# Kernel optimization log

Measured on AMD Instinct MI355X. Metric: run time of the kernel, lower is better.

## Reference

```python
import jax, jax.numpy as jnp
import numpy as np

N, E, IN_DIM, H, D = 100000, 1600000, 256, 4, 32


def setup_inputs() -> dict:
    key = jax.random.key(0)
    ks = jax.random.split(key, 12)
    glorot = lambda k, shp: jax.random.normal(k, shp, dtype=jnp.float32) * np.float32(np.sqrt(2.0 / (shp[0] + shp[1])))
    return {
        "x": jax.random.normal(ks[0], (N, IN_DIM), dtype=jnp.float32),
        "row": jnp.sort(jax.random.randint(ks[1], (E,), 0, N)),
        "col": jax.random.randint(ks[2], (E,), 0, N),
        "a1_w": glorot(ks[3], (H, IN_DIM)),
        "a1_b": jnp.zeros((H,), jnp.float32),
        "a2_w": glorot(ks[4], (H, IN_DIM)),
        "a2_b": jnp.zeros((H,), jnp.float32),
        "lin_l_w": glorot(ks[5], (H * D, IN_DIM)),
        "lin_l_b": jnp.zeros((H * D,), jnp.float32),
        "lin_r_w": glorot(ks[6], (H * D, IN_DIM)),
        "lin_r_b": jnp.zeros((H * D,), jnp.float32),
    }


def reference(x, row, col, a1_w, a1_b, a2_w, a2_b, lin_l_w, lin_l_b, lin_r_w, lin_r_b):
    n = x.shape[0]
    # per-node attention logits, gathered per edge: attn[e,h] = a1(x)[row[e],h] + a2(x)[col[e],h]
    attn1 = x @ a1_w.T + a1_b            # [N, H]
    attn2 = x @ a2_w.T + a2_b            # [N, H]
    attn = attn1[row] + attn2[col]       # [E, H]
    # segment softmax over destination node (row), numerically stable
    seg_max = jax.ops.segment_max(attn, row, num_segments=n)
    seg_max = jnp.where(jnp.isfinite(seg_max), seg_max, 0.0)  # isolated nodes
    e = jnp.exp(attn - seg_max[row])
    seg_sum = jax.ops.segment_sum(e, row, num_segments=n)
    attn_d = e / (seg_sum[row] + 1e-16)  # [E, H]
    # per-head sparse weighted aggregation: out[r] += attn_d[e] * xw[col[e]]
    xw = (x @ lin_l_w.T + lin_l_b).reshape(n, H, D)
    msg = attn_d[:, :, None] * xw[col]   # [E, H, D]
    out_l = jax.ops.segment_sum(msg, row, num_segments=n).reshape(n, H * D)
    return out_l + x @ lin_r_w.T + lin_r_b
```

## Files before the change

### kernel.cpp

```cpp
#include <hip/hip_runtime.h>
#include <hip/hip_bf16.h>
#include <math.h>

#define IN_DIM 256
#define NH 4
#define HD 128

typedef __attribute__((ext_vector_type(8))) short short8;
typedef __attribute__((ext_vector_type(4))) float floatx4;
typedef __attribute__((ext_vector_type(2))) float floatx2;

__device__ __forceinline__ unsigned short f2bf(float f) {
    __hip_bfloat16 h = __float2bfloat16(f);
    return *reinterpret_cast<unsigned short*>(&h);
}
__device__ __forceinline__ float asf(unsigned int u) {
    union { unsigned int i; float f; } c; c.i = u; return c.f;
}

__global__ __launch_bounds__(256) void setup_k(const float* __restrict__ ll_w,
                                               const float* __restrict__ lr_w,
                                               unsigned short* __restrict__ Wb,
                                               const int* __restrict__ row,
                                               int* __restrict__ rowptr,
                                               int E, int N) {
    if (blockIdx.x < 256) {
        int idx = blockIdx.x * 256 + threadIdx.x;
        int j = idx >> 8, k = idx & 255;
        float v = (j < 128) ? ll_w[(size_t)j * 256 + k] : lr_w[(size_t)(j - 128) * 256 + k];
        Wb[idx] = f2bf(v);
        return;
    }
    int e = (blockIdx.x - 256) * blockDim.x + threadIdx.x;
    if (e >= E) return;
    int r = row[e];
    int rprev = (e > 0) ? row[e - 1] : -1;
    for (int rr = rprev + 1; rr <= r; ++rr) rowptr[rr] = e;
    if (e == E - 1) {
        for (int rr = r + 1; rr <= N; ++rr) rowptr[rr] = E;
    }
}

__global__ __launch_bounds__(512, 2) void node_gemm_k(
    const float* __restrict__ x, const unsigned short* __restrict__ Wb,
    const float* __restrict__ ll_b, const float* __restrict__ lr_b,
    const float* __restrict__ a2_w, const float* __restrict__ a2_b,
    float* __restrict__ eattn,
    unsigned short* __restrict__ xwb, float* __restrict__ out, int N)
{
    __shared__ unsigned short Abuf[32 * 264];
    __shared__ unsigned short LdsX[32 * 136];
    __shared__ float          LdsO[32 * 132];

    const int tid = threadIdx.x;
    const int lane = tid & 63;
    const int w = tid >> 6;
    const int lo = lane & 15;
    const int hi = lane >> 4;

    short8 Bf[2][8];
    int cols[2]; float bias[2];
    #pragma unroll
    for (int ct = 0; ct < 2; ++ct) {
        const int col = w * 32 + ct * 16 + lo;
        cols[ct] = col;
        bias[ct] = (col < HD) ? ll_b[col] : lr_b[col - HD];
        #pragma unroll
        for (int s = 0; s < 8; ++s)
            Bf[ct][s] = *(const short8*)(Wb + (size_t)col * IN_DIM + s * 32 + hi * 8);
    }

    const int tr = tid >> 4;
    const int tq = tid & 15;

    const float ab0 = a2_b[0], ab1 = a2_b[1], ab2 = a2_b[2], ab3 = a2_b[3];

    float4 f0, f1, f2, f3;
    auto gprefetch = [&](int slab) {
        int rg = slab * 32 + tr;
        if (rg >= N) rg = 0;
        const float* px = x + (size_t)rg * IN_DIM + tq * 4;
        f0 = *(const float4*)(px);
        f1 = *(const float4*)(px + 64);
        f2 = *(const float4*)(px + 128);
        f3 = *(const float4*)(px + 192);
    };

    const int nslab = (N + 31) >> 5;
    int slab = blockIdx.x;
    gprefetch(slab);

    for (; slab < nslab; slab += gridDim.x) {
        unsigned short* ab = &Abuf[0];

        {
            ushort4 u;
            u.x = f2bf(f0.x); u.y = f2bf(f0.y); u.z = f2bf(f0.z); u.w = f2bf(f0.w);
            *(ushort4*)(ab + tr * 264 + tq * 4) = u;
            u.x = f2bf(f1.x); u.y = f2bf(f1.y); u.z = f2bf(f1.z); u.w = f2bf(f1.w);
            *(ushort4*)(ab + tr * 264 + 64 + tq * 4) = u;
            u.x = f2bf(f2.x); u.y = f2bf(f2.y); u.z = f2bf(f2.z); u.w = f2bf(f2.w);
            *(ushort4*)(ab + tr * 264 + 128 + tq * 4) = u;
            u.x = f2bf(f3.x); u.y = f2bf(f3.y); u.z = f2bf(f3.z); u.w = f2bf(f3.w);
            *(ushort4*)(ab + tr * 264 + 192 + tq * 4) = u;
        }

        float p0 = 0.f, p1 = 0.f, p2 = 0.f, p3 = 0.f;
        {
            const float* aw = a2_w + tq * 4;
            #pragma unroll
            for (int j = 0; j < 4; ++j) {
                const float4 fx = (j == 0) ? f0 : (j == 1) ? f1 : (j == 2) ? f2 : f3;
                const float4 w0v = *(const float4*)(aw + 0 * IN_DIM + j * 64);
                const float4 w1v = *(const float4*)(aw + 1 * IN_DIM + j * 64);
                const float4 w2v = *(const float4*)(aw + 2 * IN_DIM + j * 64);
                const float4 w3v = *(const float4*)(aw + 3 * IN_DIM + j * 64);
                p0 += fx.x * w0v.x + fx.y * w0v.y + fx.z * w0v.z + fx.w * w0v.w;
                p1 += fx.x * w1v.x + fx.y * w1v.y + fx.z * w1v.z + fx.w * w1v.w;
                p2 += fx.x * w2v.x + fx.y * w2v.y + fx.z * w2v.z + fx.w * w2v.w;
                p3 += fx.x * w3v.x + fx.y * w3v.y + fx.z * w3v.z + fx.w * w3v.w;
            }
        }

        asm volatile("s_waitcnt lgkmcnt(0)\n\ts_barrier" ::: "memory");

        const int next = slab + gridDim.x;
        if (next < nslab) gprefetch(next);

        #pragma unroll
        for (int o = 1; o < 16; o <<= 1) {
            p0 += __shfl_xor(p0, o, 64);
            p1 += __shfl_xor(p1, o, 64);
            p2 += __shfl_xor(p2, o, 64);
            p3 += __shfl_xor(p3, o, 64);
        }
        {
            const int rgo = slab * 32 + tr;
            if (tq == 0 && rgo < N) {
                float4 ev;
                ev.x = __expf(p0 + ab0);
                ev.y = __expf(p1 + ab1);
                ev.z = __expf(p2 + ab2);
                ev.w = __expf(p3 + ab3);
                *(float4*)(eattn + (size_t)rgo * NH) = ev;
            }
        }

        floatx4 acc[2][2];
        #pragma unroll
        for (int rt = 0; rt < 2; ++rt)
            #pragma unroll
            for (int ct = 0; ct < 2; ++ct)
                acc[rt][ct] = (floatx4){0.f, 0.f, 0.f, 0.f};

        #pragma unroll
        for (int s = 0; s < 8; ++s) {
            const short8 A0 = *(const short8*)(ab + lo * 264 + s * 32 + hi * 8);
            const short8 A1 = *(const short8*)(ab + (16 + lo) * 264 + s * 32 + hi * 8);
            acc[0][0] = __builtin_amdgcn_mfma_f32_16x16x32_bf16(A0, Bf[0][s], acc[0][0], 0, 0, 0);
            acc[0][1] = __builtin_amdgcn_mfma_f32_16x16x32_bf16(A0, Bf[1][s], acc[0][1], 0, 0, 0);
            acc[1][0] = __builtin_amdgcn_mfma_f32_16x16x32_bf16(A1, Bf[0][s], acc[1][0], 0, 0, 0);
            acc[1][1] = __builtin_amdgcn_mfma_f32_16x16x32_bf16(A1, Bf[1][s], acc[1][1], 0, 0, 0);
        }

        #pragma unroll
        for (int rt = 0; rt < 2; ++rt)
            #pragma unroll
            for (int ct = 0; ct < 2; ++ct) {
                const int c = cols[ct];
                #pragma unroll
                for (int j = 0; j < 4; ++j) {
                    const int r = rt * 16 + hi * 4 + j;
                    const float v = acc[rt][ct][j] + bias[ct];
                    if (c < HD) LdsX[r * 136 + c] = f2bf(v);
                    else        LdsO[r * 132 + (c - HD)] = v;
                }
            }

        asm volatile("s_waitcnt lgkmcnt(0)\n\ts_barrier" ::: "memory");

        {
            const int rg = slab * 32 + tr;
            if (rg < N) {
                *(uint4*)(xwb + (size_t)rg * HD + tq * 8) =
                    *(const uint4*)(LdsX + tr * 136 + tq * 8);
                float4* od = (float4*)(out + (size_t)rg * HD + tq * 8);
                const float* lsrc = LdsO + tr * 132 + tq * 8;
                od[0] = *(const float4*)(lsrc);
                od[1] = *(const float4*)(lsrc + 4);
            }
        }
    }
}

__global__ __launch_bounds__(256) void edge_aggregate_k(
    const int* __restrict__ rowptr, const int* __restrict__ col,
    const float* __restrict__ eattn,
    const unsigned short* __restrict__ xwb, float* __restrict__ out,
    int N, int E)
{
    const int n = blockIdx.x * 4 + (threadIdx.x >> 6);
    const int lane = threadIdx.x & 63;
    if (n >= N) return;
    const int e0 = __builtin_amdgcn_readfirstlane(rowptr[n]);
    const int e1 = __builtin_amdgcn_readfirstlane(rowptr[n + 1]);
    if (e0 >= e1) return;

    const int h = lane >> 4;
    const int d2 = 2 * lane;
    const int elast = E - 1;

    auto cl = [&](int i) { return col[i <= elast ? i : elast]; };

    floatx2* op = (floatx2*)(out + (size_t)n * HD + d2);
    floatx2 o = __builtin_nontemporal_load(op);

    float s = 0.f, acc0 = 0.f, acc1 = 0.f;
    int e = e0;
    int c[8];
    #pragma unroll
    for (int i = 0; i < 8; ++i) c[i] = cl(e + i);

    for (;;) {
        float wt[8];
        unsigned int pk[8];
        #pragma unroll
        for (int i = 0; i < 8; ++i) wt[i] = eattn[c[i] * NH + h];
        #pragma unroll
        for (int i = 0; i < 8; ++i)
            pk[i] = *(const unsigned int*)(xwb + (size_t)c[i] * HD + d2);
        const int ne = e + 8;
        int nx[8];
        #pragma unroll
        for (int i = 0; i < 8; ++i) nx[i] = cl(ne + i);
        #pragma unroll
        for (int i = 1; i < 8; ++i) wt[i] = (e + i < e1) ? wt[i] : 0.f;
        #pragma unroll
        for (int i = 0; i < 8; ++i) {
            s += wt[i];
            acc0 += wt[i] * asf(pk[i] << 16);
            acc1 += wt[i] * asf(pk[i] & 0xffff0000u);
        }
        if (ne >= e1) break;
        e = ne;
        #pragma unroll
        for (int i = 0; i < 8; ++i) c[i] = nx[i];
    }

    const float inv = 1.f / s;
    o.x += acc0 * inv;
    o.y += acc1 * inv;
    __builtin_nontemporal_store(o, op);
}

extern "C" void kernel_launch(void* const* d_in, const int* in_sizes, int n_in,
                              void* d_out, int out_size, void* d_ws, size_t ws_size,
                              hipStream_t stream) {
    const float* x    = (const float*)d_in[0];
    const int*   row  = (const int*)d_in[1];
    const int*   col  = (const int*)d_in[2];
    const float* a2_w = (const float*)d_in[5];
    const float* a2_b = (const float*)d_in[6];
    const float* ll_w = (const float*)d_in[7];
    const float* ll_b = (const float*)d_in[8];
    const float* lr_w = (const float*)d_in[9];
    const float* lr_b = (const float*)d_in[10];
    float* out = (float*)d_out;

    const int N = in_sizes[0] / IN_DIM;
    const int E = in_sizes[1];

    char* ws = (char*)d_ws;
    size_t off = ((size_t)(N + 1) * sizeof(int) + 255) & ~(size_t)255;
    int*   rowptr = (int*)ws;
    float* eattn  = (float*)(ws + off); off += (size_t)N * NH * sizeof(float);
    unsigned short* xwb = (unsigned short*)(ws + off); off += (size_t)N * HD * sizeof(unsigned short);
    unsigned short* Wb  = (unsigned short*)(ws + off); off += (size_t)256 * IN_DIM * sizeof(unsigned short);

    setup_k<<<256 + (E + 255) / 256, 256, 0, stream>>>(ll_w, lr_w, Wb, row, rowptr, E, N);
    node_gemm_k<<<512, 512, 0, stream>>>(x, Wb, ll_b, lr_b, a2_w, a2_b, eattn, xwb, out, N);
    edge_aggregate_k<<<(N + 3) / 4, 256, 0, stream>>>(rowptr, col, eattn, xwb, out, N, E);
}
```

Measured before the change: 282.9 us.

## Fold setup kernel into node GEMM and reorder MFMA before reductions

Removes the separate setup kernel. Each GEMM block now converts its slice of the fp32 weights to bf16 in registers, and the blocks build rowptr with a grid-stride loop over edges. The MFMA block is moved ahead of the shuffle reduction and the exp store so the two can overlap, and the grid grows from 512 to 768 blocks. This saves a kernel launch and the bf16 weight round-trip through memory. In exchange every block reloads the fp32 weights, and the rowptr loop adds work before the main loop.

Result: slower. 296.2 us (+4.7%).

```diff
diff --git a/kernel.cpp b/kernel.cpp
--- a/kernel.cpp
+++ b/kernel.cpp
@@ -18,35 +18,14 @@
     union { unsigned int i; float f; } c; c.i = u; return c.f;
 }
 
-__global__ __launch_bounds__(256) void setup_k(const float* __restrict__ ll_w,
-                                               const float* __restrict__ lr_w,
-                                               unsigned short* __restrict__ Wb,
-                                               const int* __restrict__ row,
-                                               int* __restrict__ rowptr,
-                                               int E, int N) {
-    if (blockIdx.x < 256) {
-        int idx = blockIdx.x * 256 + threadIdx.x;
-        int j = idx >> 8, k = idx & 255;
-        float v = (j < 128) ? ll_w[(size_t)j * 256 + k] : lr_w[(size_t)(j - 128) * 256 + k];
-        Wb[idx] = f2bf(v);
-        return;
-    }
-    int e = (blockIdx.x - 256) * blockDim.x + threadIdx.x;
-    if (e >= E) return;
-    int r = row[e];
-    int rprev = (e > 0) ? row[e - 1] : -1;
-    for (int rr = rprev + 1; rr <= r; ++rr) rowptr[rr] = e;
-    if (e == E - 1) {
-        for (int rr = r + 1; rr <= N; ++rr) rowptr[rr] = E;
-    }
-}
-
 __global__ __launch_bounds__(512, 2) void node_gemm_k(
-    const float* __restrict__ x, const unsigned short* __restrict__ Wb,
+    const float* __restrict__ x,
+    const float* __restrict__ ll_w, const float* __restrict__ lr_w,
     const float* __restrict__ ll_b, const float* __restrict__ lr_b,
     const float* __restrict__ a2_w, const float* __restrict__ a2_b,
+    const int* __restrict__ row, int* __restrict__ rowptr,
     float* __restrict__ eattn,
-    unsigned short* __restrict__ xwb, float* __restrict__ out, int N)
+    unsigned short* __restrict__ xwb, float* __restrict__ out, int N, int E)
 {
     __shared__ unsigned short Abuf[32 * 264];
     __shared__ unsigned short LdsX[32 * 136];
@@ -58,22 +37,8 @@
     const int lo = lane & 15;
     const int hi = lane >> 4;
 
-    short8 Bf[2][8];
-    int cols[2]; float bias[2];
-    #pragma unroll
-    for (int ct = 0; ct < 2; ++ct) {
-        const int col = w * 32 + ct * 16 + lo;
-        cols[ct] = col;
-        bias[ct] = (col < HD) ? ll_b[col] : lr_b[col - HD];
-        #pragma unroll
-        for (int s = 0; s < 8; ++s)
-            Bf[ct][s] = *(const short8*)(Wb + (size_t)col * IN_DIM + s * 32 + hi * 8);
-    }
-
     const int tr = tid >> 4;
     const int tq = tid & 15;
-
-    const float ab0 = a2_b[0], ab1 = a2_b[1], ab2 = a2_b[2], ab3 = a2_b[3];
 
     float4 f0, f1, f2, f3;
     auto gprefetch = [&](int slab) {
@@ -89,6 +54,39 @@
     const int nslab = (N + 31) >> 5;
     int slab = blockIdx.x;
     gprefetch(slab);
+
+    short8 Bf[2][8];
+    int cols[2]; float bias[2];
+    #pragma unroll
+    for (int ct = 0; ct < 2; ++ct) {
+        const int col = w * 32 + ct * 16 + lo;
+        cols[ct] = col;
+        bias[ct] = (col < HD) ? ll_b[col] : lr_b[col - HD];
+        const float* wsrc = (col < HD) ? (ll_w + (size_t)col * IN_DIM)
+                                       : (lr_w + (size_t)(col - HD) * IN_DIM);
+        #pragma unroll
+        for (int s = 0; s < 8; ++s) {
+            const float4 a = *(const float4*)(wsrc + s * 32 + hi * 8);
+            const float4 b = *(const float4*)(wsrc + s * 32 + hi * 8 + 4);
+            short8 f;
+            f[0] = (short)f2bf(a.x); f[1] = (short)f2bf(a.y);
+            f[2] = (short)f2bf(a.z); f[3] = (short)f2bf(a.w);
+            f[4] = (short)f2bf(b.x); f[5] = (short)f2bf(b.y);
+            f[6] = (short)f2bf(b.z); f[7] = (short)f2bf(b.w);
+            Bf[ct][s] = f;
+        }
+    }
+
+    for (int e = blockIdx.x * 512 + tid; e < E; e += gridDim.x * 512) {
+        const int r = row[e];
+        const int rprev = (e > 0) ? row[e - 1] : -1;
+        for (int rr = rprev + 1; rr <= r; ++rr) rowptr[rr] = e;
+        if (e == E - 1) {
+            for (int rr = r + 1; rr <= N; ++rr) rowptr[rr] = E;
+        }
+    }
+
+    const float ab0 = a2_b[0], ab1 = a2_b[1], ab2 = a2_b[2], ab3 = a2_b[3];
 
     for (; slab < nslab; slab += gridDim.x) {
         unsigned short* ab = &Abuf[0];
@@ -127,6 +125,23 @@
         const int next = slab + gridDim.x;
         if (next < nslab) gprefetch(next);
 
+        floatx4 acc[2][2];
+        #pragma unroll
+        for (int rt = 0; rt < 2; ++rt)
+            #pragma unroll
+            for (int ct = 0; ct < 2; ++ct)
+                acc[rt][ct] = (floatx4){0.f, 0.f, 0.f, 0.f};
+
+        #pragma unroll
+        for (int s = 0; s < 8; ++s) {
+            const short8 A0 = *(const short8*)(ab + lo * 264 + s * 32 + hi * 8);
+            const short8 A1 = *(const short8*)(ab + (16 + lo) * 264 + s * 32 + hi * 8);
+            acc[0][0] = __builtin_amdgcn_mfma_f32_16x16x32_bf16(A0, Bf[0][s], acc[0][0], 0, 0, 0);
+            acc[0][1] = __builtin_amdgcn_mfma_f32_16x16x32_bf16(A0, Bf[1][s], acc[0][1], 0, 0, 0);
+            acc[1][0] = __builtin_amdgcn_mfma_f32_16x16x32_bf16(A1, Bf[0][s], acc[1][0], 0, 0, 0);
+            acc[1][1] = __builtin_amdgcn_mfma_f32_16x16x32_bf16(A1, Bf[1][s], acc[1][1], 0, 0, 0);
+        }
+
         #pragma unroll
         for (int o = 1; o < 16; o <<= 1) {
             p0 += __shfl_xor(p0, o, 64);
@@ -144,23 +159,6 @@
                 ev.w = __expf(p3 + ab3);
                 *(float4*)(eattn + (size_t)rgo * NH) = ev;
             }
-        }
-
-        floatx4 acc[2][2];
-        #pragma unroll
-        for (int rt = 0; rt < 2; ++rt)
-            #pragma unroll
-            for (int ct = 0; ct < 2; ++ct)
-                acc[rt][ct] = (floatx4){0.f, 0.f, 0.f, 0.f};
-
-        #pragma unroll
-        for (int s = 0; s < 8; ++s) {
-            const short8 A0 = *(const short8*)(ab + lo * 264 + s * 32 + hi * 8);
-            const short8 A1 = *(const short8*)(ab + (16 + lo) * 264 + s * 32 + hi * 8);
-            acc[0][0] = __builtin_amdgcn_mfma_f32_16x16x32_bf16(A0, Bf[0][s], acc[0][0], 0, 0, 0);
-            acc[0][1] = __builtin_amdgcn_mfma_f32_16x16x32_bf16(A0, Bf[1][s], acc[0][1], 0, 0, 0);
-            acc[1][0] = __builtin_amdgcn_mfma_f32_16x16x32_bf16(A1, Bf[0][s], acc[1][0], 0, 0, 0);
-            acc[1][1] = __builtin_amdgcn_mfma_f32_16x16x32_bf16(A1, Bf[1][s], acc[1][1], 0, 0, 0);
         }
 
         #pragma unroll
@@ -275,9 +273,8 @@
     int*   rowptr = (int*)ws;
     float* eattn  = (float*)(ws + off); off += (size_t)N * NH * sizeof(float);
     unsigned short* xwb = (unsigned short*)(ws + off); off += (size_t)N * HD * sizeof(unsigned short);
-    unsigned short* Wb  = (unsigned short*)(ws + off); off += (size_t)256 * IN_DIM * sizeof(unsigned short);
-
-    setup_k<<<256 + (E + 255) / 256, 256, 0, stream>>>(ll_w, lr_w, Wb, row, rowptr, E, N);
-    node_gemm_k<<<512, 512, 0, stream>>>(x, Wb, ll_b, lr_b, a2_w, a2_b, eattn, xwb, out, N);
+
+    node_gemm_k<<<768, 512, 0, stream>>>(x, ll_w, lr_w, ll_b, lr_b, a2_w, a2_b,
+                                         row, rowptr, eattn, xwb, out, N, E);
     edge_aggregate_k<<<(N + 3) / 4, 256, 0, stream>>>(rowptr, col, eattn, xwb, out, N, E);
 }
```

## Store lin_r result as bf16 in workspace instead of fp32 to output

Applied to the files above, without the earlier changes.

The GEMM kernel now writes both the lin_l and lin_r projections as bf16 into a combined 256-wide workspace row, instead of writing the lin_r part as fp32 directly to the output. The aggregation kernel reads the bf16 lin_r values for its node and writes the output exactly once, with no read-modify-write. This cuts GEMM store traffic and removes the output read in the edge kernel. In exchange the skip-connection term loses precision to bf16, and gathered xw rows are now strided at 512 bytes instead of 256.

Result: no change. 278.6 us (-1.5%).

```diff
diff --git a/kernel.cpp b/kernel.cpp
--- a/kernel.cpp
+++ b/kernel.cpp
@@ -46,11 +46,10 @@
     const float* __restrict__ ll_b, const float* __restrict__ lr_b,
     const float* __restrict__ a2_w, const float* __restrict__ a2_b,
     float* __restrict__ eattn,
-    unsigned short* __restrict__ xwb, float* __restrict__ out, int N)
+    unsigned short* __restrict__ xwb, int N)
 {
     __shared__ unsigned short Abuf[32 * 264];
-    __shared__ unsigned short LdsX[32 * 136];
-    __shared__ float          LdsO[32 * 132];
+    __shared__ unsigned short LdsE[32 * 264];
 
     const int tid = threadIdx.x;
     const int lane = tid & 63;
@@ -171,9 +170,7 @@
                 #pragma unroll
                 for (int j = 0; j < 4; ++j) {
                     const int r = rt * 16 + hi * 4 + j;
-                    const float v = acc[rt][ct][j] + bias[ct];
-                    if (c < HD) LdsX[r * 136 + c] = f2bf(v);
-                    else        LdsO[r * 132 + (c - HD)] = v;
+                    LdsE[r * 264 + c] = f2bf(acc[rt][ct][j] + bias[ct]);
                 }
             }
 
@@ -182,12 +179,10 @@
         {
             const int rg = slab * 32 + tr;
             if (rg < N) {
-                *(uint4*)(xwb + (size_t)rg * HD + tq * 8) =
-                    *(const uint4*)(LdsX + tr * 136 + tq * 8);
-                float4* od = (float4*)(out + (size_t)rg * HD + tq * 8);
-                const float* lsrc = LdsO + tr * 132 + tq * 8;
-                od[0] = *(const float4*)(lsrc);
-                od[1] = *(const float4*)(lsrc + 4);
+                const uint4* lsrc = (const uint4*)(LdsE + tr * 264 + tq * 16);
+                uint4* dst = (uint4*)(xwb + (size_t)rg * 256 + tq * 16);
+                dst[0] = lsrc[0];
+                dst[1] = lsrc[1];
             }
         }
     }
@@ -204,7 +199,6 @@
     if (n >= N) return;
     const int e0 = __builtin_amdgcn_readfirstlane(rowptr[n]);
     const int e1 = __builtin_amdgcn_readfirstlane(rowptr[n + 1]);
-    if (e0 >= e1) return;
 
     const int h = lane >> 4;
     const int d2 = 2 * lane;
@@ -212,45 +206,55 @@
 
     auto cl = [&](int i) { return col[i <= elast ? i : elast]; };
 
+    const unsigned int lr = *(const unsigned int*)(xwb + (size_t)n * 256 + HD + d2);
+    const float lrx = asf(lr << 16);
+    const float lry = asf(lr & 0xffff0000u);
+
+    float2 o;
+    o.x = lrx; o.y = lry;
+
+    if (e0 < e1) {
+        float s = 0.f, acc0 = 0.f, acc1 = 0.f;
+        int e = e0;
+        int c[8];
+        #pragma unroll
+        for (int i = 0; i < 8; ++i) c[i] = cl(e + i);
+
+        for (;;) {
+            float wt[8];
+            unsigned int pk[8];
+            #pragma unroll
+            for (int i = 0; i < 8; ++i) wt[i] = eattn[c[i] * NH + h];
+            #pragma unroll
+            for (int i = 0; i < 8; ++i)
+                pk[i] = *(const unsigned int*)(xwb + (size_t)c[i] * 256 + d2);
+            const int ne = e + 8;
+            int nx[8];
+            #pragma unroll
+            for (int i = 0; i < 8; ++i) nx[i] = cl(ne + i);
+            #pragma unroll
+            for (int i = 1; i < 8; ++i) wt[i] = (e + i < e1) ? wt[i] : 0.f;
+            #pragma unroll
+            for (int i = 0; i < 8; ++i) {
+                s += wt[i];
+                acc0 += wt[i] * asf(pk[i] << 16);
+                acc1 += wt[i] * asf(pk[i] & 0xffff0000u);
+            }
+            if (ne >= e1) break;
+            e = ne;
+            #pragma unroll
+            for (int i = 0; i < 8; ++i) c[i] = nx[i];
+        }
+
+        const float inv = 1.f / s;
+        o.x += acc0 * inv;
+        o.y += acc1 * inv;
+    }
+
     floatx2* op = (floatx2*)(out + (size_t)n * HD + d2);
-    floatx2 o = __builtin_nontemporal_load(op);
-
-    float s = 0.f, acc0 = 0.f, acc1 = 0.f;
-    int e = e0;
-    int c[8];
-    #pragma unroll
-    for (int i = 0; i < 8; ++i) c[i] = cl(e + i);
-
-    for (;;) {
-        float wt[8];
-        unsigned int pk[8];
-        #pragma unroll
-        for (int i = 0; i < 8; ++i) wt[i] = eattn[c[i] * NH + h];
-        #pragma unroll
-        for (int i = 0; i < 8; ++i)
-            pk[i] = *(const unsigned int*)(xwb + (size_t)c[i] * HD + d2);
-        const int ne = e + 8;
-        int nx[8];
-        #pragma unroll
-        for (int i = 0; i < 8; ++i) nx[i] = cl(ne + i);
-        #pragma unroll
-        for (int i = 1; i < 8; ++i) wt[i] = (e + i < e1) ? wt[i] : 0.f;
-        #pragma unroll
-        for (int i = 0; i < 8; ++i) {
-            s += wt[i];
-            acc0 += wt[i] * asf(pk[i] << 16);
-            acc1 += wt[i] * asf(pk[i] & 0xffff0000u);
-        }
-        if (ne >= e1) break;
-        e = ne;
-        #pragma unroll
-        for (int i = 0; i < 8; ++i) c[i] = nx[i];
-    }
-
-    const float inv = 1.f / s;
-    o.x += acc0 * inv;
-    o.y += acc1 * inv;
-    __builtin_nontemporal_store(o, op);
+    floatx2 ov;
+    ov.x = o.x; ov.y = o.y;
+    __builtin_nontemporal_store(ov, op);
 }
 
 extern "C" void kernel_launch(void* const* d_in, const int* in_sizes, int n_in,
@@ -274,10 +278,10 @@
     size_t off = ((size_t)(N + 1) * sizeof(int) + 255) & ~(size_t)255;
     int*   rowptr = (int*)ws;
     float* eattn  = (float*)(ws + off); off += (size_t)N * NH * sizeof(float);
-    unsigned short* xwb = (unsigned short*)(ws + off); off += (size_t)N * HD * sizeof(unsigned short);
+    unsigned short* xwb = (unsigned short*)(ws + off); off += (size_t)N * 256 * sizeof(unsigned short);
     unsigned short* Wb  = (unsigned short*)(ws + off); off += (size_t)256 * IN_DIM * sizeof(unsigned short);
 
     setup_k<<<256 + (E + 255) / 256, 256, 0, stream>>>(ll_w, lr_w, Wb, row, rowptr, E, N);
-    node_gemm_k<<<512, 512, 0, stream>>>(x, Wb, ll_b, lr_b, a2_w, a2_b, eattn, xwb, out, N);
+    node_gemm_k<<<512, 512, 0, stream>>>(x, Wb, ll_b, lr_b, a2_w, a2_b, eattn, xwb, N);
     edge_aggregate_k<<<(N + 3) / 4, 256, 0, stream>>>(rowptr, col, eattn, xwb, out, N, E);
 }
```
